# Performance work log

Hardware: AMD Instinct MI355X
Metric: run time of the kernel (lower is better)

Reference implementation:

```python
import jax, jax.numpy as jnp
import numpy as np
from jax import lax

PH = PW = 7  # patch size


def _unfold2d(x, ph, pw):
    # x: [B, C, H, W] -> patches [B*Ho*Wo, C*ph*pw], channel-major like F.unfold
    B, C, H, W = x.shape
    patches = lax.conv_general_dilated_patches(
        x, filter_shape=(ph, pw), window_strides=(1, 1), padding='VALID')
    # patches: [B, C*ph*pw, Ho, Wo] with feature order (c, i, j) matching F.unfold
    Ho, Wo = H - ph + 1, W - pw + 1
    D = C * ph * pw
    q2d = patches.reshape(B, D, Ho * Wo).transpose(0, 2, 1).reshape(B * Ho * Wo, D)
    return q2d, (B, C, H, W, Ho, Wo, D)


def _fold2d_mean(res, shape_info):
    # res: [B*Ho*Wo, D] patch values -> overlap-add mean image [B, C, H, W]
    B, C, H, W, Ho, Wo, D = shape_info
    res = res.reshape(B, Ho, Wo, C, PH, PW)
    out = jnp.zeros((B, C, H, W), dtype=res.dtype)
    cnt = jnp.zeros((H, W), dtype=res.dtype)
    for di in range(PH):          # small fixed 7x7 loop over patch offsets
        for dj in range(PW):
            out = out.at[:, :, di:di + Ho, dj:dj + Wo].add(
                res[:, :, :, :, di, dj].transpose(0, 3, 1, 2))
            cnt = cnt.at[di:di + Ho, dj:dj + Wo].add(1.0)
    return out / cnt  # reduce='mean'


def setup_inputs() -> dict:
    key = jax.random.key(0)
    k1, k2, k3 = jax.random.split(key, 3)
    query = jax.random.normal(k1, (1, 3, 96, 96), dtype=jnp.float32)
    kmat = jax.random.normal(k2, (8100, 147), dtype=jnp.float32)
    vmat = jax.random.normal(k3, (8100, 147), dtype=jnp.float32)
    return {"query": query, "key": kmat, "value": vmat}


def reference(query, key, value):
    # 1) unfold query image into patch rows [Nq, D]
    q2d, shape_info = _unfold2d(query, PH, PW)
    # 2) nearest-neighbor lookup: squared-euclidean argmin over key rows
    qn = jnp.sum(q2d * q2d, axis=1, keepdims=True)        # [Nq, 1]
    kn = jnp.sum(key * key, axis=1)                       # [Nk]
    dist = qn + kn[None, :] - 2.0 * (q2d @ key.T)         # [Nq, Nk]
    idx = jnp.argmin(dist, axis=1)                        # [Nq]
    # 3) gather matched value patches and fold back (overlap-add mean)
    res = value[idx]                                      # [Nq, D]
    return _fold2d_mean(res, shape_info)
```

## Files before the change

### kernel.cpp

```cpp
#include <hip/hip_runtime.h>


#define NQ 8100
#define NK 8100
#define DD 147
#define HO 90
#define IMG 96
#define NCH 5
#define CST 262144
#define ARRN (NCH * CST)

typedef _Float16 half8 __attribute__((ext_vector_type(8)));
typedef float f32x4 __attribute__((ext_vector_type(4)));

__device__ __forceinline__ void gld16(const _Float16* g, _Float16* l) {
    __builtin_amdgcn_global_load_lds(
        (const __attribute__((address_space(1))) unsigned int*)g,
        (__attribute__((address_space(3))) unsigned int*)l, 16, 0, 0);
}

__global__ void k_prep(const float* __restrict__ query, const float* __restrict__ key,
                       _Float16* __restrict__ Qh, _Float16* __restrict__ Ql,
                       _Float16* __restrict__ Kh, _Float16* __restrict__ Kl,
                       float* __restrict__ kn, unsigned long long* __restrict__ fidx64) {
    const int bx = blockIdx.x;
    const bool isK = (blockIdx.y != 0);

    if (bx >= 640) {
        if (!isK) return;
        int wave = threadIdx.x >> 6, lane = threadIdx.x & 63;
        int kb = ((bx - 640) * 4 + wave) * 16;
        for (int r = 0; r < 16; ++r) {
            int k = kb + r;
            float s = 0.f;
            if (k < NK)
                for (int d = lane; d < DD; d += 64) {
                    float v = key[k * DD + d];
                    s += v * v;
                }
#pragma unroll
            for (int off = 32; off; off >>= 1) s += __shfl_down(s, off, 64);
            if (lane == 0) {
                kn[k] = (k < NK) ? s : 1e30f;
                fidx64[k] = 0xFFFFFFFFFFFFFFFFull;
            }
        }
        return;
    }

    int t = bx * 256 + threadIdx.x;
    int c = t >> 15;
    int rem = t & 32767;
    int col = ((rem >> 6) << 4) + (rem & 15);
    int quad = (rem >> 4) & 3;
    int kbase = c * 32 + quad * 8;

    float v[8];
#pragma unroll
    for (int j = 0; j < 8; ++j) {
        int k = kbase + j;
        float x = 0.f;
        if (k < DD && col < NQ) {
            if (isK) {
                x = key[col * DD + k];
            } else {
                int c3 = k / 49, r2 = k - 49 * c3;
                int rr = r2 / 7, ss = r2 - 7 * rr;
                int y = col / HO, xx = col - HO * y;
                x = query[(c3 * IMG + y + rr) * IMG + xx + ss];
            }
        }
        v[j] = x;
    }
    half8 h8, l8;
#pragma unroll
    for (int j = 0; j < 8; ++j) {
        _Float16 h = (_Float16)v[j];
        h8[j] = h;
        l8[j] = (_Float16)((v[j] - (float)h) * 2048.0f);
    }
    if (isK) {
        *(half8*)(Kh + t * 8) = h8;
        *(half8*)(Kl + t * 8) = l8;
    } else {
        *(half8*)(Qh + t * 8) = h8;
        *(half8*)(Ql + t * 8) = l8;
    }
}

__launch_bounds__(256, 2)
__global__ void k_nn(const _Float16* __restrict__ Qh, const _Float16* __restrict__ Ql,
                     const _Float16* __restrict__ Kh, const _Float16* __restrict__ Kl,
                     const float* __restrict__ kn, unsigned long long* __restrict__ out) {
    __shared__ __align__(16) char smem[65536];
    _Float16* sbase = (_Float16*)smem;

    const int tid = (int)threadIdx.x;
    const int wave = tid >> 6, lane = tid & 63;
    const int l15 = lane & 15, quad = lane >> 4;

    const int b = (int)blockIdx.x;
    const int xcd = b & 7;
    const int i = b >> 3;
    const int qt = (xcd >> 1) * 16 + (i & 15);
    const int kt = (xcd & 1) * 32 + (i >> 4);

    const int mbase = (wave >> 1) * 64;
    const int nbase = (wave & 1) * 64;
    const int q0 = qt * 128, n0 = kt * 128;

    const _Float16* gsrc = (wave == 0) ? Qh : (wave == 1) ? Ql : (wave == 2) ? Kh : Kl;
    const int gbase = ((wave < 2) ? qt : kt) * 8;
    const _Float16* gp0 = gsrc + gbase * 512 + lane * 8;
    _Float16* ldst0 = sbase + wave * 4096 + lane * 8;

    f32x4 acc0[4][4], acc1[4][4];
#pragma unroll
    for (int ii = 0; ii < 4; ++ii)
#pragma unroll
        for (int j = 0; j < 4; ++j) {
            acc0[ii][j] = (f32x4)0.f;
            acc1[ii][j] = (f32x4)0.f;
        }

    const int agrp = (mbase >> 4);
    const int bgrp = (nbase >> 4);

#pragma unroll
    for (int grp = 0; grp < 8; ++grp)
        gld16(gp0 + grp * 512, ldst0 + grp * 512);

#pragma unroll
    for (int c = 0; c < NCH; ++c) {
        __syncthreads();
        if (c + 1 < NCH) {
            const _Float16* gp = gp0 + (c + 1) * CST;
            _Float16* ld = ldst0 + ((c + 1) & 1) * 16384;
#pragma unroll
            for (int grp = 0; grp < 8; ++grp)
                gld16(gp + grp * 512, ld + grp * 512);
        }

        const _Float16* sQh = sbase + (c & 1) * 16384;
        const _Float16* sQl = sQh + 4096;
        const _Float16* sKh = sQh + 8192;
        const _Float16* sKl = sQh + 12288;

        half8 ah[4], al[4];
#pragma unroll
        for (int mt = 0; mt < 4; ++mt) {
            int aoff = (agrp + mt) * 512 + lane * 8;
            ah[mt] = *(const half8*)(sQh + aoff);
            al[mt] = *(const half8*)(sQl + aoff);
        }
#pragma unroll
        for (int nt = 0; nt < 4; ++nt) {
            int boff = (bgrp + nt) * 512 + lane * 8;
            half8 bh = *(const half8*)(sKh + boff);
            half8 bl = *(const half8*)(sKl + boff);
#pragma unroll
            for (int mt = 0; mt < 4; ++mt) {
                acc0[mt][nt] = __builtin_amdgcn_mfma_f32_16x16x32_f16(ah[mt], bh, acc0[mt][nt], 0, 0, 0);
                acc1[mt][nt] = __builtin_amdgcn_mfma_f32_16x16x32_f16(ah[mt], bl, acc1[mt][nt], 0, 0, 0);
                acc1[mt][nt] = __builtin_amdgcn_mfma_f32_16x16x32_f16(al[mt], bh, acc1[mt][nt], 0, 0, 0);
            }
        }
    }

    float knv[4];
    int nglob[4];
#pragma unroll
    for (int nt = 0; nt < 4; ++nt) {
        nglob[nt] = n0 + nbase + nt * 16 + l15;
        knv[nt] = kn[nglob[nt]];
    }
    __syncthreads();
    float* redv = (float*)smem;
    int* redi = (int*)(smem + 17408);

#pragma unroll
    for (int mt = 0; mt < 4; ++mt)
#pragma unroll
        for (int r = 0; r < 4; ++r) {
            float bv = 1e38f;
            int bn = 0x7fffffff;
#pragma unroll
            for (int nt = 0; nt < 4; ++nt) {
                float d = knv[nt] - 2.0f * (acc0[mt][nt][r] + acc1[mt][nt][r] * (1.0f / 2048.0f));
                if (d < bv) { bv = d; bn = nglob[nt]; }
            }
            int m = mbase + mt * 16 + quad * 4 + r;
            int cidx = (nbase >> 2) + l15;
            redv[m * 33 + cidx] = bv;
            redi[m * 33 + cidx] = bn;
        }
    __syncthreads();

    if (tid < 128) {
        float bv = 1e38f;
        int bn = 0x7fffffff;
        for (int t2 = 0; t2 < 32; ++t2) {
            float v = redv[tid * 33 + t2];
            int n = redi[tid * 33 + t2];
            if (v < bv || (v == bv && n < bn)) { bv = v; bn = n; }
        }
        unsigned u = __float_as_uint(bv);
        u = (u & 0x80000000u) ? ~u : (u | 0x80000000u);
        unsigned long long pk = ((unsigned long long)u << 32) | (unsigned)bn;
        atomicMin(&out[q0 + tid], pk);
    }
}

__global__ void k_fold(const float* __restrict__ value,
                       const unsigned long long* __restrict__ fidx64,
                       float* __restrict__ out) {
    int t = blockIdx.x * 256 + threadIdx.x;
    if (t >= 3 * IMG * IMG) return;
    int c = t / (IMG * IMG);
    int rem = t % (IMG * IMG);
    int Y = rem / IMG, X = rem % IMG;
    int i0 = max(0, Y - (HO - 1)), i1 = min(6, Y);
    int j0 = max(0, X - (HO - 1)), j1 = min(6, X);
    float s = 0.f;
    for (int i = i0; i <= i1; ++i)
        for (int j = j0; j <= j1; ++j) {
            int p = (Y - i) * HO + (X - j);
            int row = (int)(fidx64[p] & 0xFFFFFFFFull);
            s += value[row * DD + c * 49 + i * 7 + j];
        }
    float cnt = (float)((i1 - i0 + 1) * (j1 - j0 + 1));
    out[t] = s / cnt;
}

extern "C" void kernel_launch(void* const* d_in, const int* in_sizes, int n_in,
                              void* d_out, int out_size, void* d_ws, size_t ws_size,
                              hipStream_t stream) {
    const float* query = (const float*)d_in[0];
    const float* key   = (const float*)d_in[1];
    const float* value = (const float*)d_in[2];
    float* out = (float*)d_out;

    _Float16* Qh = (_Float16*)d_ws;
    _Float16* Ql = Qh + ARRN;
    _Float16* Kh = Ql + ARRN;
    _Float16* Kl = Kh + ARRN;
    float* kn = (float*)(Kl + ARRN);
    unsigned long long* fidx64 = (unsigned long long*)(kn + 8192);

    dim3 gp(768, 2);
    k_prep<<<gp, 256, 0, stream>>>(query, key, Qh, Ql, Kh, Kl, kn, fidx64);
    k_nn<<<4096, 256, 0, stream>>>(Qh, Ql, Kh, Kl, kn, fidx64);
    k_fold<<<108, 256, 0, stream>>>(value, fidx64, out);
}
```

Measured before the change: 165.2 us.

## Interleave LDS loads with MFMAs in NN kernel and unroll fold gathers

In the nearest-neighbor GEMM loop, LDS fragment loads are interleaved with MFMA issue using sched_group_barrier hints, and wave priority is raised around the compute section. This is meant to hide LDS latency behind matrix ops. Separately, the fold kernel is fully unrolled: all 49 index loads are issued first, then the value gathers, with masking instead of variable loop bounds. Its launch uses 128-thread blocks for more blocks. The fold changes add register pressure, and the unconditional gathers read index 0 for out-of-range positions.

Result: no change. 162.5 us (-1.6%).

```diff
diff --git a/kernel.cpp b/kernel.cpp
--- a/kernel.cpp
+++ b/kernel.cpp
@@ -146,15 +146,36 @@
         const _Float16* sKh = sQh + 8192;
         const _Float16* sKl = sQh + 12288;
 
+        __builtin_amdgcn_s_setprio(1);
         half8 ah[4], al[4];
-#pragma unroll
-        for (int mt = 0; mt < 4; ++mt) {
-            int aoff = (agrp + mt) * 512 + lane * 8;
-            ah[mt] = *(const half8*)(sQh + aoff);
-            al[mt] = *(const half8*)(sQl + aoff);
-        }
-#pragma unroll
-        for (int nt = 0; nt < 4; ++nt) {
+        {
+            int boff = (bgrp + 0) * 512 + lane * 8;
+            half8 bh = *(const half8*)(sKh + boff);
+            half8 bl = *(const half8*)(sKl + boff);
+            {
+                int aoff = (agrp + 0) * 512 + lane * 8;
+                ah[0] = *(const half8*)(sQh + aoff);
+                al[0] = *(const half8*)(sQl + aoff);
+                acc0[0][0] = __builtin_amdgcn_mfma_f32_16x16x32_f16(ah[0], bh, acc0[0][0], 0, 0, 0);
+                acc1[0][0] = __builtin_amdgcn_mfma_f32_16x16x32_f16(ah[0], bl, acc1[0][0], 0, 0, 0);
+                acc1[0][0] = __builtin_amdgcn_mfma_f32_16x16x32_f16(al[0], bh, acc1[0][0], 0, 0, 0);
+                __builtin_amdgcn_sched_group_barrier(0x100, 4, 0);
+                __builtin_amdgcn_sched_group_barrier(0x008, 3, 0);
+            }
+#pragma unroll
+            for (int mt = 1; mt < 4; ++mt) {
+                int aoff = (agrp + mt) * 512 + lane * 8;
+                ah[mt] = *(const half8*)(sQh + aoff);
+                al[mt] = *(const half8*)(sQl + aoff);
+                acc0[mt][0] = __builtin_amdgcn_mfma_f32_16x16x32_f16(ah[mt], bh, acc0[mt][0], 0, 0, 0);
+                acc1[mt][0] = __builtin_amdgcn_mfma_f32_16x16x32_f16(ah[mt], bl, acc1[mt][0], 0, 0, 0);
+                acc1[mt][0] = __builtin_amdgcn_mfma_f32_16x16x32_f16(al[mt], bh, acc1[mt][0], 0, 0, 0);
+                __builtin_amdgcn_sched_group_barrier(0x100, 2, 0);
+                __builtin_amdgcn_sched_group_barrier(0x008, 3, 0);
+            }
+        }
+#pragma unroll
+        for (int nt = 1; nt < 4; ++nt) {
             int boff = (bgrp + nt) * 512 + lane * 8;
             half8 bh = *(const half8*)(sKh + boff);
             half8 bl = *(const half8*)(sKl + boff);
@@ -164,7 +185,10 @@
                 acc1[mt][nt] = __builtin_amdgcn_mfma_f32_16x16x32_f16(ah[mt], bl, acc1[mt][nt], 0, 0, 0);
                 acc1[mt][nt] = __builtin_amdgcn_mfma_f32_16x16x32_f16(al[mt], bh, acc1[mt][nt], 0, 0, 0);
             }
-        }
+            __builtin_amdgcn_sched_group_barrier(0x100, 2, 0);
+            __builtin_amdgcn_sched_group_barrier(0x008, 12, 0);
+        }
+        __builtin_amdgcn_s_setprio(0);
     }
 
     float knv[4];
@@ -214,21 +238,35 @@
 __global__ void k_fold(const float* __restrict__ value,
                        const unsigned long long* __restrict__ fidx64,
                        float* __restrict__ out) {
-    int t = blockIdx.x * 256 + threadIdx.x;
+    int t = blockIdx.x * 128 + threadIdx.x;
     if (t >= 3 * IMG * IMG) return;
     int c = t / (IMG * IMG);
     int rem = t % (IMG * IMG);
     int Y = rem / IMG, X = rem % IMG;
-    int i0 = max(0, Y - (HO - 1)), i1 = min(6, Y);
-    int j0 = max(0, X - (HO - 1)), j1 = min(6, X);
-    float s = 0.f;
-    for (int i = i0; i <= i1; ++i)
-        for (int j = j0; j <= j1; ++j) {
-            int p = (Y - i) * HO + (X - j);
-            int row = (int)(fidx64[p] & 0xFFFFFFFFull);
-            s += value[row * DD + c * 49 + i * 7 + j];
-        }
-    float cnt = (float)((i1 - i0 + 1) * (j1 - j0 + 1));
+    const float* vbase = value + c * 49;
+    const unsigned* fidx32 = (const unsigned*)fidx64;
+
+    int rows[49];
+    bool oks[49];
+#pragma unroll
+    for (int i = 0; i < 7; ++i)
+#pragma unroll
+        for (int j = 0; j < 7; ++j) {
+            int yy = Y - i, xx = X - j;
+            bool ok = ((unsigned)yy < (unsigned)HO) && ((unsigned)xx < (unsigned)HO);
+            int p = ok ? (yy * HO + xx) : 0;
+            rows[i * 7 + j] = (int)fidx32[2 * p];
+            oks[i * 7 + j] = ok;
+        }
+    float s = 0.f, cnt = 0.f;
+#pragma unroll
+    for (int i = 0; i < 7; ++i)
+#pragma unroll
+        for (int j = 0; j < 7; ++j) {
+            int k = i * 7 + j;
+            float v = vbase[rows[k] * DD + k];
+            if (oks[k]) { s += v; cnt += 1.f; }
+        }
     out[t] = s / cnt;
 }
 
@@ -250,5 +288,5 @@
     dim3 gp(768, 2);
     k_prep<<<gp, 256, 0, stream>>>(query, key, Qh, Ql, Kh, Kl, kn, fidx64);
     k_nn<<<4096, 256, 0, stream>>>(Qh, Ql, Kh, Kl, kn, fidx64);
-    k_fold<<<108, 256, 0, stream>>>(value, fidx64, out);
-}
+    k_fold<<<216, 128, 0, stream>>>(value, fidx64, out);
+}
```
